# Performance work log

Measured on AMD Instinct MI355X. Metric: run time of the kernel, lower is better.

The kernel has to match this reference:

```python
import jax, jax.numpy as jnp
import numpy as np

B, LQ, LK, D, DV = 8, 2048, 2048, 128, 128


def setup_inputs() -> dict:
    key = jax.random.key(0)
    ks = jax.random.split(key, 6)
    return {
        "query": jax.random.normal(ks[0], (B, LQ, D), dtype=jnp.float32),
        "key": jax.random.normal(ks[1], (B, LK, D), dtype=jnp.float32),
        "value": jax.random.normal(ks[2], (B, LK, DV), dtype=jnp.float32),
        "Wq": jax.random.normal(ks[3], (D, D), dtype=jnp.float32) * 0.08,
        "Wk": jax.random.normal(ks[4], (D, D), dtype=jnp.float32) * 0.08,
        "Wv": jax.random.normal(ks[5], (DV, DV), dtype=jnp.float32) * 0.08,
        "attention_mask": jnp.ones((B, 1, LK), dtype=jnp.int32),
    }


def reference(query, key, value, Wq, Wk, Wv, attention_mask):
    # Linear projections (right-multiplication, as in `x @ W`)
    q = query @ Wq          # [B, lq, n_ed]
    k = key @ Wk            # [B, lk, n_ed]
    v = value @ Wv          # [B, lk, n_ev]
    scale = 1.0 / np.sqrt(q.shape[-1])
    scores = jnp.einsum("bqd,bkd->bqk", q, k) * scale  # [B, lq, lk]
    # additive mask: 0 where attend, -inf where mask==0 (broadcasts)
    mask_vals = jnp.where(attention_mask == 0, -jnp.inf, 0.0).astype(scores.dtype)
    scores = scores + mask_vals
    attn = jax.nn.softmax(scores, axis=-1)
    return attn @ v         # [B, lq, n_ev]
```

## Files before the change

kernel.cpp:

```cpp
#include <hip/hip_runtime.h>
#include <hip/hip_bf16.h>

typedef unsigned short u16;
typedef unsigned int u32;
typedef __attribute__((ext_vector_type(8))) short s8v;
typedef __attribute__((ext_vector_type(4))) float f4v;

#define B_N 8
#define L_Q 2048
#define L_K 2048
#define DIM 128
#define KT  64
#define KSPLIT 4
#define KCHUNK (L_K / KSPLIT)

__device__ __forceinline__ u16 f2bf(float f) {
  union { float f; unsigned u; } v; v.f = f;
  return (u16)((v.u + 0x7fffu + ((v.u >> 16) & 1u)) >> 16);
}
__device__ __forceinline__ u32 packbf2(float a, float b) {
  union { __hip_bfloat162 h; u32 u; } v;
  v.h = __float22bfloat162_rn(make_float2(a, b));
  return v.u;
}
__device__ __forceinline__ void async16(const u16* g, u16* l) {
  __builtin_amdgcn_global_load_lds(
      (const __attribute__((address_space(1))) u32*)(const void*)g,
      (__attribute__((address_space(3))) u32*)(void*)l, 16, 0, 0);
}


__global__ __launch_bounds__(256) void proj_mfma(
    const float* __restrict__ query, const float* __restrict__ key,
    const float* __restrict__ value, const float* __restrict__ Wq,
    const float* __restrict__ Wk, const float* __restrict__ Wv,
    u16* __restrict__ qp, u16* __restrict__ kp, u16* __restrict__ vp) {
  __shared__ __align__(16) u16 Wf[32 * 520];
  __shared__ __align__(16) u16 Fb[8192];
  const int tid = threadIdx.x;
  const int bi = blockIdx.x;
  const int which = bi >> 8;
  const int sub = bi & 255;
  const int b = sub >> 5;
  const int rt = sub & 31;
  const float* X = (which == 0) ? query : (which == 1) ? key : value;
  const float* W = (which == 0) ? Wq : (which == 1) ? Wk : Wv;
  const float wscale = (which == 0) ? (1.44269504089f / 11.3137084990f) : 1.0f;

#pragma unroll
  for (int i = 0; i < 16; ++i) {
    int f4i = tid + i * 256;
    float4 w4 = *(const float4*)(W + f4i * 4);
    int k = f4i >> 5, col = (f4i & 31) * 4;
    int ks = k >> 5, qd = (k & 31) >> 3, j = k & 7;
    float wv[4] = {w4.x, w4.y, w4.z, w4.w};
#pragma unroll
    for (int c = 0; c < 4; ++c) {
      int n = col + c;
      Wf[(ks * 8 + (n >> 4)) * 520 + (qd * 16 + (n & 15)) * 8 + j] = f2bf(wv[c] * wscale);
    }
  }
  __syncthreads();

  const int w = tid >> 6, lane = tid & 63;
  const int ln = lane & 15, quad = lane >> 4;
  const int xrow = rt * 64 + w * 16 + ln;
  const float* Xr = X + ((size_t)b * L_Q + xrow) * DIM;

  s8v a[4];
#pragma unroll
  for (int ks = 0; ks < 4; ++ks) {
    float4 xa = *(const float4*)(Xr + ks * 32 + quad * 8);
    float4 xb = *(const float4*)(Xr + ks * 32 + quad * 8 + 4);
    s8v t;
    t[0] = (short)f2bf(xa.x); t[1] = (short)f2bf(xa.y);
    t[2] = (short)f2bf(xa.z); t[3] = (short)f2bf(xa.w);
    t[4] = (short)f2bf(xb.x); t[5] = (short)f2bf(xb.y);
    t[6] = (short)f2bf(xb.z); t[7] = (short)f2bf(xb.w);
    a[ks] = t;
  }

  f4v acc[8];
#pragma unroll
  for (int i = 0; i < 8; ++i) acc[i] = (f4v){0.f, 0.f, 0.f, 0.f};
  const u16* Wl0 = Wf + lane * 8;
#pragma unroll
  for (int ks = 0; ks < 4; ++ks)
#pragma unroll
    for (int nt = 0; nt < 8; ++nt) {
      s8v bw = *(const s8v*)(Wl0 + (ks * 8 + nt) * 520);
      acc[nt] = __builtin_amdgcn_mfma_f32_16x16x32_bf16(a[ks], bw, acc[nt], 0, 0, 0);
    }

  if (which < 2) {
#pragma unroll
    for (int nt = 0; nt < 8; ++nt) {
      int ks = nt >> 1;
      int f = (which == 0) ? (w * 4 + ks) : (ks * 4 + w);
      int lp = ((nt & 1) * 2 + (ln >> 3)) * 16;
      int j = ln & 7;
#pragma unroll
      for (int r = 0; r < 4; ++r)
        Fb[f * 512 + (lp + quad * 4 + r) * 8 + j] = f2bf(acc[nt][r]);
    }
  } else {
#pragma unroll
    for (int nt = 0; nt < 8; ++nt) {
      int f = (w >> 1) * 8 + nt;
      int lp = ((w & 1) * 2 + (quad >> 1)) * 16 + ln;
      int jb = (quad & 1) * 4;
#pragma unroll
      for (int r = 0; r < 4; ++r)
        Fb[f * 512 + lp * 8 + jb + r] = f2bf(acc[nt][r]);
    }
  }
  __syncthreads();

  u16* Y = (which == 0) ? qp + (size_t)(b * 512 + rt * 16) * 512
         : (which == 1) ? kp + (size_t)((b * 32 + rt) * 16) * 512
                        : vp + (size_t)((b * 32 + rt) * 16) * 512;
#pragma unroll
  for (int r = 0; r < 4; ++r) {
    int c = tid + r * 256;
    *(s8v*)(Y + c * 8) = *(const s8v*)(Fb + c * 8);
  }
}

__global__ __launch_bounds__(256, 4) void flash_split(
    const u16* __restrict__ qp, const u16* __restrict__ kp,
    const u16* __restrict__ vp, const int* __restrict__ mask,
    float* __restrict__ po, float* __restrict__ ml) {
  __shared__ __align__(16) u16 Kf[8192];
  __shared__ __align__(16) u16 Vf[8192];
  __shared__ float biasl[KT];

  const int tid = threadIdx.x;
  const int bi = blockIdx.x;
  const int b = bi & 7;
  const int rest = bi >> 3;
  const int p = rest & 3;
  const int qb = rest >> 2;
  const int w = tid >> 6;
  const int lane = tid & 63;
  const int ln = lane & 15;
  const int quad = lane >> 4;

  const int* mb = mask + b * L_K;

  const u16* Qt = qp + ((size_t)(b * 128 + qb * 4 + w) * 4) * 512;
  s8v aq[4];
#pragma unroll
  for (int ks = 0; ks < 4; ++ks)
    aq[ks] = *(const s8v*)(Qt + ks * 512 + lane * 8);

  f4v o[8];
#pragma unroll
  for (int i = 0; i < 8; ++i) o[i] = (f4v){0.f, 0.f, 0.f, 0.f};
  float mrow = -__builtin_inff();
  float lrow = 0.f;

  const u16* Kl0 = Kf + lane * 8;
  const u16* Vl0 = Vf + lane * 8;
  u16* Pw = Kf + w * 1024;
  const u16* Pl0 = Pw + lane * 8;

  for (int it = 0; it < KCHUNK / KT; ++it) {
    const int kt = p * (KCHUNK / KT) + it;
    const int k0 = kt * KT;
    const u16* Ktile = kp + (size_t)((b * 32 + kt) * 16) * 512;
    const u16* Vtile = vp + (size_t)((b * 32 + kt) * 16) * 512;
#pragma unroll
    for (int c = 0; c < 4; ++c) {
      int cg = w * 4 + c;
      async16(Ktile + (size_t)(cg * 64 + lane) * 8, Kf + cg * 512);
      async16(Vtile + (size_t)(cg * 64 + lane) * 8, Vf + cg * 512);
    }
    int mv = mb[k0 + lane];
    bool allones = (__ballot(mv != 0) == ~0ull);
    if (!allones && tid < KT) biasl[tid] = (mv == 0) ? -__builtin_inff() : 0.f;
    __syncthreads();

    f4v s[4];
#pragma unroll
    for (int mt = 0; mt < 4; ++mt) s[mt] = (f4v){0.f, 0.f, 0.f, 0.f};
#pragma unroll
    for (int ks = 0; ks < 4; ++ks)
#pragma unroll
      for (int mt = 0; mt < 4; ++mt) {
        s8v bk = *(const s8v*)(Kl0 + (ks * 4 + mt) * 512);
        s[mt] = __builtin_amdgcn_mfma_f32_16x16x32_bf16(bk, aq[ks], s[mt], 0, 0, 0);
      }
    if (!allones) {
#pragma unroll
      for (int mt = 0; mt < 4; ++mt) {
        float4 bt = *(const float4*)&biasl[mt * 16 + quad * 4];
        s[mt][0] += bt.x; s[mt][1] += bt.y; s[mt][2] += bt.z; s[mt][3] += bt.w;
      }
    }
    float m16 = s[0][0];
#pragma unroll
    for (int mt = 0; mt < 4; ++mt)
#pragma unroll
      for (int r = 0; r < 4; ++r) m16 = fmaxf(m16, s[mt][r]);
    m16 = fmaxf(m16, __shfl_xor(m16, 16, 64));
    m16 = fmaxf(m16, __shfl_xor(m16, 32, 64));

    float mn = fmaxf(mrow, m16);
    float alpha = __builtin_amdgcn_exp2f(fminf(mrow - mn, 0.f));
    mrow = mn;
    float rs = 0.f;
#pragma unroll
    for (int mt = 0; mt < 4; ++mt)
#pragma unroll
      for (int r = 0; r < 4; ++r) {
        s[mt][r] = __builtin_amdgcn_exp2f(fminf(s[mt][r] - mn, 0.f));
        rs += s[mt][r];
      }
    rs += __shfl_xor(rs, 16, 64);
    rs += __shfl_xor(rs, 32, 64);
    lrow = lrow * alpha + rs;

    __syncthreads();

#pragma unroll
    for (int mt = 0; mt < 4; ++mt) {
      int base = (mt >> 1) * 512 + (((mt & 1) * 2 + (quad >> 1)) * 16 + ln) * 8 + (quad & 1) * 4;
      *(u32*)(Pw + base)     = packbf2(s[mt][0], s[mt][1]);
      *(u32*)(Pw + base + 2) = packbf2(s[mt][2], s[mt][3]);
    }

    float ar[4];
#pragma unroll
    for (int r = 0; r < 4; ++r) ar[r] = __shfl(alpha, quad * 4 + r, 64);
#pragma unroll
    for (int n2 = 0; n2 < 8; ++n2)
#pragma unroll
      for (int r = 0; r < 4; ++r) o[n2][r] *= ar[r];

#pragma unroll
    for (int kv = 0; kv < 2; ++kv) {
      s8v ap = *(const s8v*)(Pl0 + kv * 512);
#pragma unroll
      for (int n2 = 0; n2 < 8; ++n2) {
        s8v bv = *(const s8v*)(Vl0 + (kv * 8 + n2) * 512);
        o[n2] = __builtin_amdgcn_mfma_f32_16x16x32_bf16(ap, bv, o[n2], 0, 0, 0);
      }
    }
    __syncthreads();
  }

#pragma unroll
  for (int n2 = 0; n2 < 8; ++n2)
#pragma unroll
    for (int r = 0; r < 4; ++r) {
      size_t q = (size_t)b * L_Q + qb * 64 + w * 16 + quad * 4 + r;
      po[(q * KSPLIT + p) * DIM + n2 * 16 + ln] = o[n2][r];
    }
  if (quad == 0) {
    size_t q = (size_t)b * L_Q + qb * 64 + w * 16 + ln;
    *(float2*)&ml[(q * KSPLIT + p) * 2] = make_float2(mrow, lrow);
  }
}

__global__ __launch_bounds__(256) void combine(
    const float* __restrict__ po, const float* __restrict__ ml,
    float* __restrict__ out) {
  const int t = threadIdx.x;
  const int lr = t >> 5, l32 = t & 31;
  const size_t q = (size_t)blockIdx.x * 8 + lr;

  float m[KSPLIT], l[KSPLIT];
#pragma unroll
  for (int p = 0; p < KSPLIT; ++p) {
    m[p] = ml[(q * KSPLIT + p) * 2 + 0];
    l[p] = ml[(q * KSPLIT + p) * 2 + 1];
  }
  float M = m[0];
#pragma unroll
  for (int p = 1; p < KSPLIT; ++p) M = fmaxf(M, m[p]);
  float wp[KSPLIT], L = 0.f;
#pragma unroll
  for (int p = 0; p < KSPLIT; ++p) {
    wp[p] = __builtin_amdgcn_exp2f(fminf(m[p] - M, 0.f));
    L += l[p] * wp[p];
  }
  float invL = 1.0f / L;

  float4 acc = make_float4(0.f, 0.f, 0.f, 0.f);
#pragma unroll
  for (int p = 0; p < KSPLIT; ++p) {
    float4 v = *(const float4*)(po + (q * KSPLIT + p) * DIM + l32 * 4);
    acc.x += wp[p] * v.x; acc.y += wp[p] * v.y;
    acc.z += wp[p] * v.z; acc.w += wp[p] * v.w;
  }
  acc.x *= invL; acc.y *= invL; acc.z *= invL; acc.w *= invL;
  *(float4*)(out + q * DIM + l32 * 4) = acc;
}

extern "C" void kernel_launch(void* const* d_in, const int* in_sizes, int n_in,
                              void* d_out, int out_size, void* d_ws, size_t ws_size,
                              hipStream_t stream) {
  const float* query = (const float*)d_in[0];
  const float* key   = (const float*)d_in[1];
  const float* value = (const float*)d_in[2];
  const float* Wq    = (const float*)d_in[3];
  const float* Wk    = (const float*)d_in[4];
  const float* Wv    = (const float*)d_in[5];
  const int*   mask  = (const int*)d_in[6];
  float* out = (float*)d_out;

  u16* qp = (u16*)d_ws;
  u16* kp = qp + (size_t)B_N * L_Q * DIM;
  u16* vp = kp + (size_t)B_N * L_K * DIM;
  float* po = (float*)(vp + (size_t)B_N * DIM * L_K);
  float* ml = po + (size_t)B_N * L_Q * KSPLIT * DIM;

  hipLaunchKernelGGL(proj_mfma, dim3(768), dim3(256), 0, stream,
                     query, key, value, Wq, Wk, Wv, qp, kp, vp);
  hipLaunchKernelGGL(flash_split, dim3(1024), dim3(256), 0, stream,
                     qp, kp, vp, mask, po, ml);
  hipLaunchKernelGGL(combine, dim3((B_N * L_Q) / 8), dim3(256), 0, stream,
                     po, ml, out);
}
```

Measured before the change: 121.2 us.

## Switch attention to 32x32 MFMA with register P, bf16 partials, precomputed weights

```diff
diff --git a/kernel.cpp b/kernel.cpp
--- a/kernel.cpp
+++ b/kernel.cpp
@@ -5,6 +5,7 @@
 typedef unsigned int u32;
 typedef __attribute__((ext_vector_type(8))) short s8v;
 typedef __attribute__((ext_vector_type(4))) float f4v;
+typedef __attribute__((ext_vector_type(16))) float f16v;
 
 #define B_N 8
 #define L_Q 2048
@@ -18,6 +19,9 @@
   union { float f; unsigned u; } v; v.f = f;
   return (u16)((v.u + 0x7fffu + ((v.u >> 16) & 1u)) >> 16);
 }
+__device__ __forceinline__ float bf2f(u16 u) {
+  union { u32 u; float f; } v; v.u = ((u32)u) << 16; return v.f;
+}
 __device__ __forceinline__ u32 packbf2(float a, float b) {
   union { __hip_bfloat162 h; u32 u; } v;
   v.h = __float22bfloat162_rn(make_float2(a, b));
@@ -30,12 +34,33 @@
 }
 
 
+__global__ __launch_bounds__(256) void wprep(
+    const float* __restrict__ Wq, const float* __restrict__ Wk,
+    const float* __restrict__ Wv, u16* __restrict__ wbuf) {
+  const int which = blockIdx.x;
+  const int tid = threadIdx.x;
+  const float* W = (which == 0) ? Wq : (which == 1) ? Wk : Wv;
+  const float wscale = (which == 0) ? (1.44269504089f / 11.3137084990f) : 1.0f;
+  u16* dst = wbuf + which * 16384;
+#pragma unroll
+  for (int i = 0; i < 16; ++i) {
+    int f4i = tid + i * 256;
+    float4 w4 = *(const float4*)(W + f4i * 4);
+    int k = f4i >> 5, col = (f4i & 31) * 4;
+    int ks = k >> 5, qd = (k & 31) >> 3, j = k & 7;
+    float wv4[4] = {w4.x, w4.y, w4.z, w4.w};
+#pragma unroll
+    for (int c = 0; c < 4; ++c) {
+      int n = col + c;
+      dst[(ks * 8 + (n >> 4)) * 512 + (qd * 16 + (n & 15)) * 8 + j] = f2bf(wv4[c] * wscale);
+    }
+  }
+}
+
 __global__ __launch_bounds__(256) void proj_mfma(
     const float* __restrict__ query, const float* __restrict__ key,
-    const float* __restrict__ value, const float* __restrict__ Wq,
-    const float* __restrict__ Wk, const float* __restrict__ Wv,
+    const float* __restrict__ value, const u16* __restrict__ wbuf,
     u16* __restrict__ qp, u16* __restrict__ kp, u16* __restrict__ vp) {
-  __shared__ __align__(16) u16 Wf[32 * 520];
   __shared__ __align__(16) u16 Fb[8192];
   const int tid = threadIdx.x;
   const int bi = blockIdx.x;
@@ -44,23 +69,7 @@
   const int b = sub >> 5;
   const int rt = sub & 31;
   const float* X = (which == 0) ? query : (which == 1) ? key : value;
-  const float* W = (which == 0) ? Wq : (which == 1) ? Wk : Wv;
-  const float wscale = (which == 0) ? (1.44269504089f / 11.3137084990f) : 1.0f;
-
-#pragma unroll
-  for (int i = 0; i < 16; ++i) {
-    int f4i = tid + i * 256;
-    float4 w4 = *(const float4*)(W + f4i * 4);
-    int k = f4i >> 5, col = (f4i & 31) * 4;
-    int ks = k >> 5, qd = (k & 31) >> 3, j = k & 7;
-    float wv[4] = {w4.x, w4.y, w4.z, w4.w};
-#pragma unroll
-    for (int c = 0; c < 4; ++c) {
-      int n = col + c;
-      Wf[(ks * 8 + (n >> 4)) * 520 + (qd * 16 + (n & 15)) * 8 + j] = f2bf(wv[c] * wscale);
-    }
-  }
-  __syncthreads();
+  const u16* Wfg = wbuf + which * 16384;
 
   const int w = tid >> 6, lane = tid & 63;
   const int ln = lane & 15, quad = lane >> 4;
@@ -83,42 +92,32 @@
   f4v acc[8];
 #pragma unroll
   for (int i = 0; i < 8; ++i) acc[i] = (f4v){0.f, 0.f, 0.f, 0.f};
-  const u16* Wl0 = Wf + lane * 8;
 #pragma unroll
   for (int ks = 0; ks < 4; ++ks)
 #pragma unroll
     for (int nt = 0; nt < 8; ++nt) {
-      s8v bw = *(const s8v*)(Wl0 + (ks * 8 + nt) * 520);
+      s8v bw = *(const s8v*)(Wfg + (ks * 8 + nt) * 512 + lane * 8);
       acc[nt] = __builtin_amdgcn_mfma_f32_16x16x32_bf16(a[ks], bw, acc[nt], 0, 0, 0);
     }
 
   if (which < 2) {
 #pragma unroll
     for (int nt = 0; nt < 8; ++nt) {
-      int ks = nt >> 1;
-      int f = (which == 0) ? (w * 4 + ks) : (ks * 4 + w);
-      int lp = ((nt & 1) * 2 + (ln >> 3)) * 16;
-      int j = ln & 7;
-#pragma unroll
-      for (int r = 0; r < 4; ++r)
-        Fb[f * 512 + (lp + quad * 4 + r) * 8 + j] = f2bf(acc[nt][r]);
+      int base = ((w >> 1) * 8 + nt) * 512 + ((ln >> 3) * 32 + (w & 1) * 16 + quad * 4) * 8 + (ln & 7);
+#pragma unroll
+      for (int r = 0; r < 4; ++r) Fb[base + r * 8] = f2bf(acc[nt][r]);
     }
   } else {
 #pragma unroll
     for (int nt = 0; nt < 8; ++nt) {
-      int f = (w >> 1) * 8 + nt;
-      int lp = ((w & 1) * 2 + (quad >> 1)) * 16 + ln;
-      int jb = (quad & 1) * 4;
-#pragma unroll
-      for (int r = 0; r < 4; ++r)
-        Fb[f * 512 + lp * 8 + jb + r] = f2bf(acc[nt][r]);
+      int base = (w * 4 + (nt >> 1)) * 512 + ((quad >> 1) * 32 + (nt & 1) * 16 + ln) * 8 + (quad & 1) * 4;
+      *(u32*)&Fb[base]     = packbf2(acc[nt][0], acc[nt][1]);
+      *(u32*)&Fb[base + 2] = packbf2(acc[nt][2], acc[nt][3]);
     }
   }
   __syncthreads();
 
-  u16* Y = (which == 0) ? qp + (size_t)(b * 512 + rt * 16) * 512
-         : (which == 1) ? kp + (size_t)((b * 32 + rt) * 16) * 512
-                        : vp + (size_t)((b * 32 + rt) * 16) * 512;
+  u16* Y = ((which == 0) ? qp : (which == 1) ? kp : vp) + (size_t)(b * 32 + rt) * 8192;
 #pragma unroll
   for (int r = 0; r < 4; ++r) {
     int c = tid + r * 256;
@@ -126,12 +125,13 @@
   }
 }
 
-__global__ __launch_bounds__(256, 4) void flash_split(
+__global__ __launch_bounds__(128, 2) void flash_split(
     const u16* __restrict__ qp, const u16* __restrict__ kp,
     const u16* __restrict__ vp, const int* __restrict__ mask,
-    float* __restrict__ po, float* __restrict__ ml) {
+    u16* __restrict__ po, float* __restrict__ ml) {
   __shared__ __align__(16) u16 Kf[8192];
   __shared__ __align__(16) u16 Vf[8192];
+  __shared__ float alphaL[2][32];
   __shared__ float biasl[KT];
 
   const int tid = threadIdx.x;
@@ -140,69 +140,70 @@
   const int rest = bi >> 3;
   const int p = rest & 3;
   const int qb = rest >> 2;
-  const int w = tid >> 6;
+  const int w2 = tid >> 6;
   const int lane = tid & 63;
-  const int ln = lane & 15;
-  const int quad = lane >> 4;
+  const int qcol = lane & 31;
+  const int H = lane >> 5;
+  const bool Hb = (H != 0);
 
   const int* mb = mask + b * L_K;
 
-  const u16* Qt = qp + ((size_t)(b * 128 + qb * 4 + w) * 4) * 512;
-  s8v aq[4];
-#pragma unroll
-  for (int ks = 0; ks < 4; ++ks)
-    aq[ks] = *(const s8v*)(Qt + ks * 512 + lane * 8);
-
-  f4v o[8];
-#pragma unroll
-  for (int i = 0; i < 8; ++i) o[i] = (f4v){0.f, 0.f, 0.f, 0.f};
+  const u16* Qt = qp + (size_t)(b * 64 + qb * 2 + w2) * 4096;
+  s8v aq[8];
+#pragma unroll
+  for (int c = 0; c < 8; ++c) aq[c] = *(const s8v*)(Qt + c * 512 + lane * 8);
+
+  f16v o[4];
+#pragma unroll
+  for (int i = 0; i < 4; ++i)
+#pragma unroll
+    for (int r = 0; r < 16; ++r) o[i][r] = 0.f;
   float mrow = -__builtin_inff();
   float lrow = 0.f;
-
-  const u16* Kl0 = Kf + lane * 8;
-  const u16* Vl0 = Vf + lane * 8;
-  u16* Pw = Kf + w * 1024;
-  const u16* Pl0 = Pw + lane * 8;
 
   for (int it = 0; it < KCHUNK / KT; ++it) {
     const int kt = p * (KCHUNK / KT) + it;
     const int k0 = kt * KT;
-    const u16* Ktile = kp + (size_t)((b * 32 + kt) * 16) * 512;
-    const u16* Vtile = vp + (size_t)((b * 32 + kt) * 16) * 512;
-#pragma unroll
-    for (int c = 0; c < 4; ++c) {
-      int cg = w * 4 + c;
-      async16(Ktile + (size_t)(cg * 64 + lane) * 8, Kf + cg * 512);
-      async16(Vtile + (size_t)(cg * 64 + lane) * 8, Vf + cg * 512);
+    const u16* Ktile = kp + (size_t)(b * 32 + kt) * 8192;
+    const u16* Vtile = vp + (size_t)(b * 32 + kt) * 8192;
+#pragma unroll
+    for (int c8 = 0; c8 < 8; ++c8) {
+      int f = w2 * 8 + c8;
+      async16(Ktile + (size_t)(f * 64 + lane) * 8, Kf + f * 512);
+      async16(Vtile + (size_t)(f * 64 + lane) * 8, Vf + f * 512);
     }
     int mv = mb[k0 + lane];
     bool allones = (__ballot(mv != 0) == ~0ull);
     if (!allones && tid < KT) biasl[tid] = (mv == 0) ? -__builtin_inff() : 0.f;
     __syncthreads();
 
-    f4v s[4];
-#pragma unroll
-    for (int mt = 0; mt < 4; ++mt) s[mt] = (f4v){0.f, 0.f, 0.f, 0.f};
-#pragma unroll
-    for (int ks = 0; ks < 4; ++ks)
-#pragma unroll
-      for (int mt = 0; mt < 4; ++mt) {
-        s8v bk = *(const s8v*)(Kl0 + (ks * 4 + mt) * 512);
-        s[mt] = __builtin_amdgcn_mfma_f32_16x16x32_bf16(bk, aq[ks], s[mt], 0, 0, 0);
-      }
+    f16v s[2];
+#pragma unroll
+    for (int t = 0; t < 2; ++t)
+#pragma unroll
+      for (int r = 0; r < 16; ++r) s[t][r] = 0.f;
+#pragma unroll
+    for (int c = 0; c < 8; ++c) {
+      s8v k0f = *(const s8v*)(Kf + c * 512 + lane * 8);
+      s[0] = __builtin_amdgcn_mfma_f32_32x32x16_bf16(k0f, aq[c], s[0], 0, 0, 0);
+      s8v k1f = *(const s8v*)(Kf + (8 + c) * 512 + lane * 8);
+      s[1] = __builtin_amdgcn_mfma_f32_32x32x16_bf16(k1f, aq[c], s[1], 0, 0, 0);
+    }
     if (!allones) {
 #pragma unroll
-      for (int mt = 0; mt < 4; ++mt) {
-        float4 bt = *(const float4*)&biasl[mt * 16 + quad * 4];
-        s[mt][0] += bt.x; s[mt][1] += bt.y; s[mt][2] += bt.z; s[mt][3] += bt.w;
-      }
+      for (int t = 0; t < 2; ++t)
+#pragma unroll
+        for (int g = 0; g < 4; ++g) {
+          float4 bt = *(const float4*)&biasl[t * 32 + g * 8 + 4 * H];
+#pragma unroll
+          for (int i = 0; i < 4; ++i) s[t][g * 4 + i] += bt.x * (i == 0) + bt.y * (i == 1) + bt.z * (i == 2) + bt.w * (i == 3);
+        }
     }
     float m16 = s[0][0];
 #pragma unroll
-    for (int mt = 0; mt < 4; ++mt)
-#pragma unroll
-      for (int r = 0; r < 4; ++r) m16 = fmaxf(m16, s[mt][r]);
-    m16 = fmaxf(m16, __shfl_xor(m16, 16, 64));
+    for (int t = 0; t < 2; ++t)
+#pragma unroll
+      for (int r = 0; r < 16; ++r) m16 = fmaxf(m16, s[t][r]);
     m16 = fmaxf(m16, __shfl_xor(m16, 32, 64));
 
     float mn = fmaxf(mrow, m16);
@@ -210,60 +211,75 @@
     mrow = mn;
     float rs = 0.f;
 #pragma unroll
-    for (int mt = 0; mt < 4; ++mt)
-#pragma unroll
-      for (int r = 0; r < 4; ++r) {
-        s[mt][r] = __builtin_amdgcn_exp2f(fminf(s[mt][r] - mn, 0.f));
-        rs += s[mt][r];
+    for (int t = 0; t < 2; ++t)
+#pragma unroll
+      for (int r = 0; r < 16; ++r) {
+        s[t][r] = __builtin_amdgcn_exp2f(fminf(s[t][r] - mn, 0.f));
+        rs += s[t][r];
       }
-    rs += __shfl_xor(rs, 16, 64);
     rs += __shfl_xor(rs, 32, 64);
     lrow = lrow * alpha + rs;
 
+    if (H == 0) alphaL[w2][qcol] = alpha;
+
+    u32 plo[2][4], phi[2][4];
+#pragma unroll
+    for (int t = 0; t < 2; ++t)
+#pragma unroll
+      for (int g = 0; g < 4; ++g) {
+        plo[t][g] = packbf2(s[t][g * 4 + 0], s[t][g * 4 + 1]);
+        phi[t][g] = packbf2(s[t][g * 4 + 2], s[t][g * 4 + 3]);
+      }
+
+#pragma unroll
+    for (int g = 0; g < 4; ++g) {
+      float4 av = *(const float4*)&alphaL[w2][g * 8 + 4 * H];
+      float a4[4] = {av.x, av.y, av.z, av.w};
+#pragma unroll
+      for (int ntv = 0; ntv < 4; ++ntv)
+#pragma unroll
+        for (int i = 0; i < 4; ++i) o[ntv][g * 4 + i] *= a4[i];
+    }
+
+#pragma unroll
+    for (int kc = 0; kc < 4; ++kc) {
+      const int t = kc >> 1, gl = (kc & 1) * 2;
+      u32 a_lo0 = plo[t][gl], a_hi0 = phi[t][gl];
+      u32 a_lo1 = plo[t][gl + 1], a_hi1 = phi[t][gl + 1];
+      u32 snd_lo = Hb ? a_lo0 : a_lo1;
+      u32 snd_hi = Hb ? a_hi0 : a_hi1;
+      u32 r_lo = (u32)__shfl_xor((int)snd_lo, 32, 64);
+      u32 r_hi = (u32)__shfl_xor((int)snd_hi, 32, 64);
+      union { u32 wd[4]; s8v v; } pa;
+      pa.wd[0] = Hb ? r_lo : a_lo0;
+      pa.wd[1] = Hb ? r_hi : a_hi0;
+      pa.wd[2] = Hb ? a_lo1 : r_lo;
+      pa.wd[3] = Hb ? a_hi1 : r_hi;
+#pragma unroll
+      for (int ntv = 0; ntv < 4; ++ntv) {
+        s8v bv = *(const s8v*)(Vf + (kc * 4 + ntv) * 512 + lane * 8);
+        o[ntv] = __builtin_amdgcn_mfma_f32_32x32x16_bf16(pa.v, bv, o[ntv], 0, 0, 0);
+      }
+    }
     __syncthreads();
-
-#pragma unroll
-    for (int mt = 0; mt < 4; ++mt) {
-      int base = (mt >> 1) * 512 + (((mt & 1) * 2 + (quad >> 1)) * 16 + ln) * 8 + (quad & 1) * 4;
-      *(u32*)(Pw + base)     = packbf2(s[mt][0], s[mt][1]);
-      *(u32*)(Pw + base + 2) = packbf2(s[mt][2], s[mt][3]);
-    }
-
-    float ar[4];
-#pragma unroll
-    for (int r = 0; r < 4; ++r) ar[r] = __shfl(alpha, quad * 4 + r, 64);
-#pragma unroll
-    for (int n2 = 0; n2 < 8; ++n2)
-#pragma unroll
-      for (int r = 0; r < 4; ++r) o[n2][r] *= ar[r];
-
-#pragma unroll
-    for (int kv = 0; kv < 2; ++kv) {
-      s8v ap = *(const s8v*)(Pl0 + kv * 512);
-#pragma unroll
-      for (int n2 = 0; n2 < 8; ++n2) {
-        s8v bv = *(const s8v*)(Vl0 + (kv * 8 + n2) * 512);
-        o[n2] = __builtin_amdgcn_mfma_f32_16x16x32_bf16(ap, bv, o[n2], 0, 0, 0);
-      }
-    }
-    __syncthreads();
-  }
-
-#pragma unroll
-  for (int n2 = 0; n2 < 8; ++n2)
-#pragma unroll
-    for (int r = 0; r < 4; ++r) {
-      size_t q = (size_t)b * L_Q + qb * 64 + w * 16 + quad * 4 + r;
-      po[(q * KSPLIT + p) * DIM + n2 * 16 + ln] = o[n2][r];
-    }
-  if (quad == 0) {
-    size_t q = (size_t)b * L_Q + qb * 64 + w * 16 + ln;
+  }
+
+#pragma unroll
+  for (int ntv = 0; ntv < 4; ++ntv)
+#pragma unroll
+    for (int reg = 0; reg < 16; ++reg) {
+      int qloc = (reg & 3) + 8 * (reg >> 2) + 4 * H;
+      size_t q = (size_t)b * L_Q + qb * 64 + w2 * 32 + qloc;
+      po[(q * KSPLIT + p) * DIM + ntv * 32 + qcol] = f2bf(o[ntv][reg]);
+    }
+  if (H == 0) {
+    size_t q = (size_t)b * L_Q + qb * 64 + w2 * 32 + qcol;
     *(float2*)&ml[(q * KSPLIT + p) * 2] = make_float2(mrow, lrow);
   }
 }
 
 __global__ __launch_bounds__(256) void combine(
-    const float* __restrict__ po, const float* __restrict__ ml,
+    const u16* __restrict__ po, const float* __restrict__ ml,
     float* __restrict__ out) {
   const int t = threadIdx.x;
   const int lr = t >> 5, l32 = t & 31;
@@ -289,9 +305,9 @@
   float4 acc = make_float4(0.f, 0.f, 0.f, 0.f);
 #pragma unroll
   for (int p = 0; p < KSPLIT; ++p) {
-    float4 v = *(const float4*)(po + (q * KSPLIT + p) * DIM + l32 * 4);
-    acc.x += wp[p] * v.x; acc.y += wp[p] * v.y;
-    acc.z += wp[p] * v.z; acc.w += wp[p] * v.w;
+    ushort4 u = *(const ushort4*)(po + (q * KSPLIT + p) * DIM + l32 * 4);
+    acc.x += wp[p] * bf2f(u.x); acc.y += wp[p] * bf2f(u.y);
+    acc.z += wp[p] * bf2f(u.z); acc.w += wp[p] * bf2f(u.w);
   }
   acc.x *= invL; acc.y *= invL; acc.z *= invL; acc.w *= invL;
   *(float4*)(out + q * DIM + l32 * 4) = acc;
@@ -312,12 +328,14 @@
   u16* qp = (u16*)d_ws;
   u16* kp = qp + (size_t)B_N * L_Q * DIM;
   u16* vp = kp + (size_t)B_N * L_K * DIM;
-  float* po = (float*)(vp + (size_t)B_N * DIM * L_K);
-  float* ml = po + (size_t)B_N * L_Q * KSPLIT * DIM;
-
+  u16* po = vp + (size_t)B_N * DIM * L_K;
+  float* ml = (float*)(po + (size_t)B_N * L_Q * KSPLIT * DIM);
+  u16* wbuf = (u16*)(ml + (size_t)B_N * L_Q * KSPLIT * 2);
+
+  hipLaunchKernelGGL(wprep, dim3(3), dim3(256), 0, stream, Wq, Wk, Wv, wbuf);
   hipLaunchKernelGGL(proj_mfma, dim3(768), dim3(256), 0, stream,
-                     query, key, value, Wq, Wk, Wv, qp, kp, vp);
-  hipLaunchKernelGGL(flash_split, dim3(1024), dim3(256), 0, stream,
+                     query, key, value, wbuf, qp, kp, vp);
+  hipLaunchKernelGGL(flash_split, dim3(1024), dim3(128), 0, stream,
                      qp, kp, vp, mask, po, ml);
   hipLaunchKernelGGL(combine, dim3((B_N * L_Q) / 8), dim3(256), 0, stream,
                      po, ml, out);
```

After: 126.7 us. 4.5% more time.
